# Performance work log

Measured on AMD Instinct MI355X. Metric: run time of the kernel, lower is better.

The kernel has to match this reference:

```python
import jax, jax.numpy as jnp
import numpy as np

NUM_TAGS = 64
SEQ_LEN = 512
BATCH = 512


def setup_inputs() -> dict:
    key = jax.random.key(0)
    k1, k2, k3, k4, k5 = jax.random.split(key, 5)
    emissions = jax.random.normal(k1, (SEQ_LEN, BATCH, NUM_TAGS), dtype=jnp.float32)
    tags = jax.random.randint(k2, (SEQ_LEN, BATCH), 0, NUM_TAGS, dtype=jnp.int32)
    mask = jnp.ones((SEQ_LEN, BATCH), dtype=jnp.int32)
    start_transitions = jax.random.uniform(k3, (NUM_TAGS,), dtype=jnp.float32)
    end_transitions = jax.random.uniform(k4, (NUM_TAGS,), dtype=jnp.float32)
    transitions = jax.random.uniform(k5, (NUM_TAGS, NUM_TAGS), dtype=jnp.float32)
    return {
        "emissions": emissions,
        "tags": tags,
        "mask": mask,
        "start_transitions": start_transitions,
        "end_transitions": end_transitions,
        "transitions": transitions,
    }


def _compute_score(emissions, tags, mask, start_transitions, end_transitions, transitions):
    # emissions: (S,B,T), tags/mask: (S,B)
    seq_length, batch_size = tags.shape
    maskf = mask.astype(jnp.float32)
    barange = jnp.arange(batch_size)
    # emission scores for gold tags at every step: (S,B)
    emit = jnp.take_along_axis(emissions, tags[:, :, None], axis=2)[:, :, 0]
    # transition scores between consecutive gold tags: (S-1,B)
    trans = transitions[tags[:-1], tags[1:]]
    score = start_transitions[tags[0]] + emit[0]
    score = score + ((trans + emit[1:]) * maskf[1:]).sum(axis=0)
    seq_ends = mask.astype(jnp.int32).sum(axis=0) - 1  # (B,)
    last_tags = tags[seq_ends, barange]
    score = score + end_transitions[last_tags]
    return score  # (B,)


def _compute_normalizer(emissions, mask, start_transitions, end_transitions, transitions):
    # sequential forward-algorithm scan over time
    score0 = start_transitions + emissions[0]  # (B,T)

    def step(score, inp):
        em, m = inp  # em: (B,T), m: (B,)
        # (B,Tprev,Tnext) logsumexp over Tprev
        next_score = jax.nn.logsumexp(
            score[:, :, None] + transitions[None, :, :] + em[:, None, :], axis=1
        )
        score = jnp.where(m[:, None].astype(bool), next_score, score)
        return score, None

    score, _ = jax.lax.scan(step, score0, (emissions[1:], mask[1:]))
    return jax.nn.logsumexp(score + end_transitions, axis=1)  # (B,)


def reference(emissions, tags, mask, start_transitions, end_transitions, transitions):
    numerator = _compute_score(emissions, tags, mask, start_transitions, end_transitions, transitions)
    denominator = _compute_normalizer(emissions, mask, start_transitions, end_transitions, transitions)
    llh = numerator - denominator
    return llh.sum()  # reduction='sum'
```

## Files before the change

### kernel.cpp

```cpp
#include <hip/hip_runtime.h>

#define T   512
#define B   512
#define NT  64
#define QS  16
#define NQ  (T / QS)
#define RING 4

typedef _Float16 h2 __attribute__((ext_vector_type(2)));

__device__ __forceinline__ float rflf(float x) {
    return __uint_as_float(__builtin_amdgcn_readfirstlane(__float_as_uint(x)));
}

__device__ __forceinline__ float dot2(h2 a, h2 b, float c) {
#if __has_builtin(__builtin_amdgcn_fdot2)
    return __builtin_amdgcn_fdot2(a, b, c, false);
#else
    return c + (float)a.x * (float)b.x + (float)a.y * (float)b.y;
#endif
}

__device__ __forceinline__ h2 bch2(int u) { return __builtin_bit_cast(h2, u); }

__global__ __launch_bounds__(64) void crf_fused(
    const float* __restrict__ emissions,
    const int*   __restrict__ tags,
    const int*   __restrict__ mask,
    const float* __restrict__ startT,
    const float* __restrict__ endT,
    const float* __restrict__ trans,
    float* __restrict__ out)
{
    const int j = threadIdx.x;

    __shared__ __align__(16) float ebuf[RING][QS][NT];

    if (blockIdx.x < B) {
        const int b = blockIdx.x;

        h2 Eh[NT / 2];
#pragma unroll
        for (int m = 0; m < NT / 2; ++m) {
            Eh[m].x = (_Float16)__expf(trans[(2 * m)     * NT + j]);
            Eh[m].y = (_Float16)__expf(trans[(2 * m + 1) * NT + j]);
        }

        const int jr = j >> 4;
        const int c0 = (j & 15) * 4;
        float4 sA[4];

        auto issue_q = [&](int g) {
#pragma unroll
            for (int k = 0; k < 4; ++k) {
                const int t = g * QS + 4 * k + jr;
                sA[k] = *(const float4*)&emissions[((size_t)t * B + b) * NT + c0];
            }
        };
        auto write_q = [&](int g) {
#pragma unroll
            for (int k = 0; k < 4; ++k) {
                float4 w;
                w.x = __expf(sA[k].x); w.y = __expf(sA[k].y);
                w.z = __expf(sA[k].z); w.w = __expf(sA[k].w);
                *(float4*)&ebuf[g & (RING - 1)][4 * k + jr][c0] = w;
            }
        };

        for (int g = 0; g < 3; ++g) { issue_q(g); write_q(g); }
        issue_q(3);

        const float e0  = emissions[(size_t)b * NT + j];
        const float sc0 = startT[j] + e0;
        const float S0  = rflf(sc0);
        float q = __expf(sc0 - S0);
        int   K = 0;

        int pk_i;
        {
            const int qi = __float_as_int(q);
            const int qo = __builtin_amdgcn_update_dpp(0, qi, 0xB1, 0xF, 0xF, true);
            pk_i = __builtin_bit_cast(int,
                    __builtin_amdgcn_cvt_pkrtz(q, __int_as_float(qo)));
        }

        float* eflat = &ebuf[0][0][0];
        int bits_prev;
        int mpre = mask[j * B + b];
        unsigned long long mbc = 0;

        {
            int u[32];
#pragma unroll
            for (int n = 0; n < 32; ++n)
                u[n] = __builtin_amdgcn_readlane(pk_i, 2 * n);
            float a[8] = {0.f, 0.f, 0.f, 0.f, 0.f, 0.f, 0.f, 0.f};
#pragma unroll
            for (int n = 0; n < 32; ++n)
                a[n & 7] = dot2(bch2(u[n]), Eh[n], a[n & 7]);
            const float p = ((a[0] + a[1]) + (a[2] + a[3]))
                          + ((a[4] + a[5]) + (a[6] + a[7]));
            bits_prev = __builtin_amdgcn_readfirstlane(__float_as_int(p));
            const int  k = ((bits_prev >> 23) & 255) - 127;
            const float r = __int_as_float((125 - k) << 23);
            const float X1 = eflat[NT + j];
            const int  m1 = mask[B + b];
            if (m1) { q = (p * X1) * r; K = k + 2; }
            const int qo = __builtin_amdgcn_update_dpp(0, __float_as_int(q),
                                                       0xB1, 0xF, 0xF, true);
            pk_i = __builtin_bit_cast(int,
                    __builtin_amdgcn_cvt_pkrtz(q, __int_as_float(qo)));
        }

        float Xc = eflat[2 * NT + j];
        float Xn = eflat[3 * NT + j];

        auto stepF = [&](int s) {
            int u[32];
#pragma unroll
            for (int n = 0; n < 32; ++n)
                u[n] = __builtin_amdgcn_readlane(pk_i, 2 * n);
            __builtin_amdgcn_sched_barrier(0);
            const int  k = ((bits_prev >> 23) & 255) - 127;
            const float r = __int_as_float((125 - k) << 23);
            K += k + 2;
            float a[8] = {0.f, 0.f, 0.f, 0.f, 0.f, 0.f, 0.f, 0.f};
#pragma unroll
            for (int n = 0; n < 32; ++n)
                a[n & 7] = dot2(bch2(u[n]), Eh[n], a[n & 7]);
            const float sXr = Xc * r;
            const float p = ((a[0] + a[1]) + (a[2] + a[3]))
                          + ((a[4] + a[5]) + (a[6] + a[7]));
            q = p * sXr;
            bits_prev = __builtin_amdgcn_readfirstlane(__float_as_int(p));
            const int qo = __builtin_amdgcn_update_dpp(0, __float_as_int(q),
                                                       0xB1, 0xF, 0xF, true);
            pk_i = __builtin_bit_cast(int,
                    __builtin_amdgcn_cvt_pkrtz(q, __int_as_float(qo)));
            Xc = Xn;
            Xn = eflat[((s + 2) & 63) * NT + j];
        };

        auto stepM = [&](int s) {
            int u[32];
#pragma unroll
            for (int n = 0; n < 32; ++n)
                u[n] = __builtin_amdgcn_readlane(pk_i, 2 * n);
            __builtin_amdgcn_sched_barrier(0);
            const int  k = ((bits_prev >> 23) & 255) - 127;
            const float r = __int_as_float((125 - k) << 23);
            const bool mc = (mbc >> (s & 63)) & 1ull;
            const float mf = mc ? 1.0f : 0.0f;
            K += mc ? (k + 2) : 0;
            float a[8] = {0.f, 0.f, 0.f, 0.f, 0.f, 0.f, 0.f, 0.f};
#pragma unroll
            for (int n = 0; n < 32; ++n)
                a[n & 7] = dot2(bch2(u[n]), Eh[n], a[n & 7]);
            const float sXr = Xc * r;
            const float p = ((a[0] + a[1]) + (a[2] + a[3]))
                          + ((a[4] + a[5]) + (a[6] + a[7]));
            const float qn = p * sXr;
            q = fmaf(mf, qn - q, q);
            bits_prev = __builtin_amdgcn_readfirstlane(__float_as_int(p));
            const int qo = __builtin_amdgcn_update_dpp(0, __float_as_int(q),
                                                       0xB1, 0xF, 0xF, true);
            pk_i = __builtin_bit_cast(int,
                    __builtin_amdgcn_cvt_pkrtz(q, __int_as_float(qo)));
            Xc = Xn;
            Xn = eflat[((s + 2) & 63) * NT + j];
        };

        for (int x = 0; x < NQ; ++x) {
            const int gw = (x + 3 < NQ) ? x + 3 : NQ - 1;
            write_q(gw);
            const int gl = (x + 4 < NQ) ? x + 4 : NQ - 1;
            issue_q(gl);

            if ((x & 3) == 0) {
                mbc = __ballot(mpre != 0);
                const int cn = ((x >> 2) + 1 < 8) ? (x >> 2) + 1 : 7;
                mpre = mask[(cn * 64 + j) * B + b];
            }

            const unsigned qb = (unsigned)(mbc >> ((x & 3) << 4)) & 0xFFFFu;
            const int tt0 = (x == 0) ? 2 : 0;

            if (qb == 0xFFFFu) {
#pragma unroll 1
                for (int tt = tt0; tt < QS; ++tt) stepF(x * QS + tt);
            } else {
#pragma unroll 1
                for (int tt = tt0; tt < QS; ++tt) stepM(x * QS + tt);
            }
        }

        float v = q * __expf(endT[j]);
#pragma unroll
        for (int off = 32; off > 0; off >>= 1)
            v += __shfl_xor(v, off);
        if (j == 0)
            atomicAdd(out, -(S0 + (float)K * 0.69314718f + __logf(v)));

    } else {
        const int b = blockIdx.x - B;

        float acc = 0.f;
        int   cnt = 0;
#pragma unroll
        for (int m = 0; m < T / 64; ++m) {
            const int t  = j + 64 * m;
            const int mv = mask[t * B + b];
            const int tg = tags[t * B + b];
            cnt += (int)__popcll(__ballot(mv != 0));
            if (t == 0) {
                acc += startT[tg] + emissions[(size_t)b * NT + tg];
            } else if (mv) {
                const int tp = tags[(t - 1) * B + b];
                acc += trans[tp * NT + tg]
                     + emissions[(size_t)(t * B + b) * NT + tg];
            }
        }
#pragma unroll
        for (int off = 32; off > 0; off >>= 1)
            acc += __shfl_xor(acc, off);
        if (j == 0) {
            const int last = tags[(size_t)(cnt - 1) * B + b];
            atomicAdd(out, acc + endT[last]);
        }
    }
}

extern "C" void kernel_launch(void* const* d_in, const int* in_sizes, int n_in,
                              void* d_out, int out_size, void* d_ws, size_t ws_size,
                              hipStream_t stream) {
    const float* emissions = (const float*)d_in[0];
    const int*   tags      = (const int*)  d_in[1];
    const int*   mask      = (const int*)  d_in[2];
    const float* startT    = (const float*)d_in[3];
    const float* endT      = (const float*)d_in[4];
    const float* trans     = (const float*)d_in[5];
    float* out = (float*)d_out;

    hipMemsetAsync(out, 0, sizeof(float), stream);
    crf_fused<<<2 * B, 64, 0, stream>>>(
        emissions, tags, mask, startT, endT, trans, out);
}
```

Before: 193.4 us.

## Split forward scan into forward/backward halves meeting at midpoint

```diff
diff --git a/kernel.cpp b/kernel.cpp
--- a/kernel.cpp
+++ b/kernel.cpp
@@ -5,6 +5,7 @@
 #define NT  64
 #define QS  16
 #define NQ  (T / QS)
+#define FNQ 16
 #define RING 4
 
 typedef _Float16 h2 __attribute__((ext_vector_type(2)));
@@ -12,7 +13,6 @@
 __device__ __forceinline__ float rflf(float x) {
     return __uint_as_float(__builtin_amdgcn_readfirstlane(__float_as_uint(x)));
 }
-
 __device__ __forceinline__ float dot2(h2 a, h2 b, float c) {
 #if __has_builtin(__builtin_amdgcn_fdot2)
     return __builtin_amdgcn_fdot2(a, b, c, false);
@@ -20,20 +20,25 @@
     return c + (float)a.x * (float)b.x + (float)a.y * (float)b.y;
 #endif
 }
-
-__device__ __forceinline__ h2 bch2(int u) { return __builtin_bit_cast(h2, u); }
-
-__global__ __launch_bounds__(64) void crf_fused(
+__device__ __forceinline__ h2  bch2(int u) { return __builtin_bit_cast(h2, u); }
+__device__ __forceinline__ int cvtpk(float a, float b) {
+    return __builtin_bit_cast(int, __builtin_amdgcn_cvt_pkrtz(a, b));
+}
+
+__global__ __launch_bounds__(64) void crf_main(
     const float* __restrict__ emissions,
     const int*   __restrict__ tags,
     const int*   __restrict__ mask,
     const float* __restrict__ startT,
     const float* __restrict__ endT,
     const float* __restrict__ trans,
+    float* __restrict__ wqf,
+    float* __restrict__ wqb,
+    float* __restrict__ wsf,
+    float* __restrict__ wsb,
     float* __restrict__ out)
 {
     const int j = threadIdx.x;
-
     __shared__ __align__(16) float ebuf[RING][QS][NT];
 
     if (blockIdx.x < B) {
@@ -49,7 +54,6 @@
         const int jr = j >> 4;
         const int c0 = (j & 15) * 4;
         float4 sA[4];
-
         auto issue_q = [&](int g) {
 #pragma unroll
             for (int k = 0; k < 4; ++k) {
@@ -66,7 +70,6 @@
                 *(float4*)&ebuf[g & (RING - 1)][4 * k + jr][c0] = w;
             }
         };
-
         for (int g = 0; g < 3; ++g) { issue_q(g); write_q(g); }
         issue_q(3);
 
@@ -75,15 +78,12 @@
         const float S0  = rflf(sc0);
         float q = __expf(sc0 - S0);
         int   K = 0;
-
         int pk_i;
         {
             const int qi = __float_as_int(q);
             const int qo = __builtin_amdgcn_update_dpp(0, qi, 0xB1, 0xF, 0xF, true);
-            pk_i = __builtin_bit_cast(int,
-                    __builtin_amdgcn_cvt_pkrtz(q, __int_as_float(qo)));
-        }
-
+            pk_i = cvtpk(q, __int_as_float(qo));
+        }
         float* eflat = &ebuf[0][0][0];
         int bits_prev;
         int mpre = mask[j * B + b];
@@ -92,100 +92,80 @@
         {
             int u[32];
 #pragma unroll
-            for (int n = 0; n < 32; ++n)
-                u[n] = __builtin_amdgcn_readlane(pk_i, 2 * n);
-            float a[8] = {0.f, 0.f, 0.f, 0.f, 0.f, 0.f, 0.f, 0.f};
-#pragma unroll
-            for (int n = 0; n < 32; ++n)
-                a[n & 7] = dot2(bch2(u[n]), Eh[n], a[n & 7]);
-            const float p = ((a[0] + a[1]) + (a[2] + a[3]))
-                          + ((a[4] + a[5]) + (a[6] + a[7]));
+            for (int m = 0; m < 32; ++m) u[m] = __builtin_amdgcn_readlane(pk_i, 2 * m);
+            float a[8] = {0.f,0.f,0.f,0.f,0.f,0.f,0.f,0.f};
+#pragma unroll
+            for (int m = 0; m < 32; ++m) a[m & 7] = dot2(bch2(u[m]), Eh[m], a[m & 7]);
+            const float p = ((a[0]+a[1])+(a[2]+a[3])) + ((a[4]+a[5])+(a[6]+a[7]));
             bits_prev = __builtin_amdgcn_readfirstlane(__float_as_int(p));
             const int  k = ((bits_prev >> 23) & 255) - 127;
             const float r = __int_as_float((125 - k) << 23);
             const float X1 = eflat[NT + j];
             const int  m1 = mask[B + b];
             if (m1) { q = (p * X1) * r; K = k + 2; }
-            const int qo = __builtin_amdgcn_update_dpp(0, __float_as_int(q),
-                                                       0xB1, 0xF, 0xF, true);
-            pk_i = __builtin_bit_cast(int,
-                    __builtin_amdgcn_cvt_pkrtz(q, __int_as_float(qo)));
-        }
-
+            const int qo = __builtin_amdgcn_update_dpp(0, __float_as_int(q), 0xB1, 0xF, 0xF, true);
+            pk_i = cvtpk(q, __int_as_float(qo));
+        }
         float Xc = eflat[2 * NT + j];
         float Xn = eflat[3 * NT + j];
 
         auto stepF = [&](int s) {
             int u[32];
 #pragma unroll
-            for (int n = 0; n < 32; ++n)
-                u[n] = __builtin_amdgcn_readlane(pk_i, 2 * n);
+            for (int m = 0; m < 32; ++m) u[m] = __builtin_amdgcn_readlane(pk_i, 2 * m);
             __builtin_amdgcn_sched_barrier(0);
             const int  k = ((bits_prev >> 23) & 255) - 127;
             const float r = __int_as_float((125 - k) << 23);
             K += k + 2;
-            float a[8] = {0.f, 0.f, 0.f, 0.f, 0.f, 0.f, 0.f, 0.f};
-#pragma unroll
-            for (int n = 0; n < 32; ++n)
-                a[n & 7] = dot2(bch2(u[n]), Eh[n], a[n & 7]);
+            float a[8] = {0.f,0.f,0.f,0.f,0.f,0.f,0.f,0.f};
+#pragma unroll
+            for (int m = 0; m < 32; ++m) a[m & 7] = dot2(bch2(u[m]), Eh[m], a[m & 7]);
             const float sXr = Xc * r;
-            const float p = ((a[0] + a[1]) + (a[2] + a[3]))
-                          + ((a[4] + a[5]) + (a[6] + a[7]));
+            const float p = ((a[0]+a[1])+(a[2]+a[3])) + ((a[4]+a[5])+(a[6]+a[7]));
             q = p * sXr;
             bits_prev = __builtin_amdgcn_readfirstlane(__float_as_int(p));
-            const int qo = __builtin_amdgcn_update_dpp(0, __float_as_int(q),
-                                                       0xB1, 0xF, 0xF, true);
-            pk_i = __builtin_bit_cast(int,
-                    __builtin_amdgcn_cvt_pkrtz(q, __int_as_float(qo)));
+            const int qo = __builtin_amdgcn_update_dpp(0, __float_as_int(q), 0xB1, 0xF, 0xF, true);
+            pk_i = cvtpk(q, __int_as_float(qo));
             Xc = Xn;
             Xn = eflat[((s + 2) & 63) * NT + j];
         };
-
         auto stepM = [&](int s) {
             int u[32];
 #pragma unroll
-            for (int n = 0; n < 32; ++n)
-                u[n] = __builtin_amdgcn_readlane(pk_i, 2 * n);
+            for (int m = 0; m < 32; ++m) u[m] = __builtin_amdgcn_readlane(pk_i, 2 * m);
             __builtin_amdgcn_sched_barrier(0);
             const int  k = ((bits_prev >> 23) & 255) - 127;
             const float r = __int_as_float((125 - k) << 23);
             const bool mc = (mbc >> (s & 63)) & 1ull;
             const float mf = mc ? 1.0f : 0.0f;
             K += mc ? (k + 2) : 0;
-            float a[8] = {0.f, 0.f, 0.f, 0.f, 0.f, 0.f, 0.f, 0.f};
-#pragma unroll
-            for (int n = 0; n < 32; ++n)
-                a[n & 7] = dot2(bch2(u[n]), Eh[n], a[n & 7]);
+            float a[8] = {0.f,0.f,0.f,0.f,0.f,0.f,0.f,0.f};
+#pragma unroll
+            for (int m = 0; m < 32; ++m) a[m & 7] = dot2(bch2(u[m]), Eh[m], a[m & 7]);
             const float sXr = Xc * r;
-            const float p = ((a[0] + a[1]) + (a[2] + a[3]))
-                          + ((a[4] + a[5]) + (a[6] + a[7]));
+            const float p = ((a[0]+a[1])+(a[2]+a[3])) + ((a[4]+a[5])+(a[6]+a[7]));
             const float qn = p * sXr;
             q = fmaf(mf, qn - q, q);
             bits_prev = __builtin_amdgcn_readfirstlane(__float_as_int(p));
-            const int qo = __builtin_amdgcn_update_dpp(0, __float_as_int(q),
-                                                       0xB1, 0xF, 0xF, true);
-            pk_i = __builtin_bit_cast(int,
-                    __builtin_amdgcn_cvt_pkrtz(q, __int_as_float(qo)));
+            const int qo = __builtin_amdgcn_update_dpp(0, __float_as_int(q), 0xB1, 0xF, 0xF, true);
+            pk_i = cvtpk(q, __int_as_float(qo));
             Xc = Xn;
             Xn = eflat[((s + 2) & 63) * NT + j];
         };
 
-        for (int x = 0; x < NQ; ++x) {
-            const int gw = (x + 3 < NQ) ? x + 3 : NQ - 1;
+        for (int x = 0; x < FNQ; ++x) {
+            const int gw = (x + 3 < FNQ) ? x + 3 : FNQ - 1;
             write_q(gw);
-            const int gl = (x + 4 < NQ) ? x + 4 : NQ - 1;
+            const int gl = (x + 4 < FNQ) ? x + 4 : FNQ - 1;
             issue_q(gl);
-
             if ((x & 3) == 0) {
                 mbc = __ballot(mpre != 0);
-                const int cn = ((x >> 2) + 1 < 8) ? (x >> 2) + 1 : 7;
+                const int cn = ((x >> 2) + 1 < 4) ? (x >> 2) + 1 : 3;
                 mpre = mask[(cn * 64 + j) * B + b];
             }
-
-            const unsigned qb = (unsigned)(mbc >> ((x & 3) << 4)) & 0xFFFFu;
+            const unsigned qb16 = (unsigned)(mbc >> ((x & 3) << 4)) & 0xFFFFu;
             const int tt0 = (x == 0) ? 2 : 0;
-
-            if (qb == 0xFFFFu) {
+            if (qb16 == 0xFFFFu) {
 #pragma unroll 1
                 for (int tt = tt0; tt < QS; ++tt) stepF(x * QS + tt);
             } else {
@@ -193,17 +173,138 @@
                 for (int tt = tt0; tt < QS; ++tt) stepM(x * QS + tt);
             }
         }
-
-        float v = q * __expf(endT[j]);
-#pragma unroll
-        for (int off = 32; off > 0; off >>= 1)
-            v += __shfl_xor(v, off);
-        if (j == 0)
-            atomicAdd(out, -(S0 + (float)K * 0.69314718f + __logf(v)));
+        wqf[b * 64 + j] = q;
+        if (j == 0) wsf[b] = S0 + (float)K * 0.69314718f;
+
+    } else if (blockIdx.x < 2 * B) {
+        const int b = blockIdx.x - B;
+
+        h2 Er[NT / 2];
+#pragma unroll
+        for (int m = 0; m < NT / 2; ++m) {
+            Er[m].x = (_Float16)__expf(trans[j * NT + 2 * m]);
+            Er[m].y = (_Float16)__expf(trans[j * NT + 2 * m + 1]);
+        }
+
+        const int jr = j >> 4;
+        const int c0 = (j & 15) * 4;
+        float4 sA[4];
+        auto issue_q = [&](int g) {
+#pragma unroll
+            for (int k = 0; k < 4; ++k) {
+                const int t = g * QS + 4 * k + jr;
+                sA[k] = *(const float4*)&emissions[((size_t)t * B + b) * NT + c0];
+            }
+        };
+        auto write_q = [&](int g) {
+#pragma unroll
+            for (int k = 0; k < 4; ++k) {
+                float4 w;
+                w.x = __expf(sA[k].x); w.y = __expf(sA[k].y);
+                w.z = __expf(sA[k].z); w.w = __expf(sA[k].w);
+                *(float4*)&ebuf[g & (RING - 1)][4 * k + jr][c0] = w;
+            }
+        };
+        for (int g = 31; g > 28; --g) { issue_q(g); write_q(g); }
+        issue_q(28);
+
+        float v = __expf(endT[j]);
+        int   K = 0;
+        float* eflat = &ebuf[0][0][0];
+        int bits_prev;
+        int mpre = mask[(7 * 64 + j) * B + b];
+        unsigned long long mbc = 0;
+        int pk_i;
+        {
+            const float y  = v * eflat[63 * NT + j];
+            const int  yo = __builtin_amdgcn_update_dpp(0, __float_as_int(y), 0xB1, 0xF, 0xF, true);
+            pk_i = cvtpk(y, __int_as_float(yo));
+        }
+        {
+            int u[32];
+#pragma unroll
+            for (int m = 0; m < 32; ++m) u[m] = __builtin_amdgcn_readlane(pk_i, 2 * m);
+            float a[8] = {0.f,0.f,0.f,0.f,0.f,0.f,0.f,0.f};
+#pragma unroll
+            for (int m = 0; m < 32; ++m) a[m & 7] = dot2(bch2(u[m]), Er[m], a[m & 7]);
+            const float p = ((a[0]+a[1])+(a[2]+a[3])) + ((a[4]+a[5])+(a[6]+a[7]));
+            bits_prev = __builtin_amdgcn_readfirstlane(__float_as_int(p));
+            const int  k = ((bits_prev >> 23) & 255) - 127;
+            const float r = __int_as_float((125 - k) << 23);
+            const int  m511 = mask[511 * B + b];
+            if (m511) { v = p * r; K = k + 2; }
+            const float y  = v * eflat[62 * NT + j];
+            const int  yo = __builtin_amdgcn_update_dpp(0, __float_as_int(y), 0xB1, 0xF, 0xF, true);
+            pk_i = cvtpk(y, __int_as_float(yo));
+        }
+
+        auto bstepF = [&](int s) {
+            int u[32];
+#pragma unroll
+            for (int m = 0; m < 32; ++m) u[m] = __builtin_amdgcn_readlane(pk_i, 2 * m);
+            __builtin_amdgcn_sched_barrier(0);
+            const int  k = ((bits_prev >> 23) & 255) - 127;
+            const float r = __int_as_float((125 - k) << 23);
+            K += k + 2;
+            float a[8] = {0.f,0.f,0.f,0.f,0.f,0.f,0.f,0.f};
+#pragma unroll
+            for (int m = 0; m < 32; ++m) a[m & 7] = dot2(bch2(u[m]), Er[m], a[m & 7]);
+            const float Xn = eflat[((s - 1) & 63) * NT + j];
+            const float p = ((a[0]+a[1])+(a[2]+a[3])) + ((a[4]+a[5])+(a[6]+a[7]));
+            v = p * r;
+            bits_prev = __builtin_amdgcn_readfirstlane(__float_as_int(p));
+            const float y  = v * Xn;
+            const int  yo = __builtin_amdgcn_update_dpp(0, __float_as_int(y), 0xB1, 0xF, 0xF, true);
+            pk_i = cvtpk(y, __int_as_float(yo));
+        };
+        auto bstepM = [&](int s) {
+            int u[32];
+#pragma unroll
+            for (int m = 0; m < 32; ++m) u[m] = __builtin_amdgcn_readlane(pk_i, 2 * m);
+            __builtin_amdgcn_sched_barrier(0);
+            const int  k = ((bits_prev >> 23) & 255) - 127;
+            const float r = __int_as_float((125 - k) << 23);
+            const bool mc = (mbc >> (s & 63)) & 1ull;
+            const float mf = mc ? 1.0f : 0.0f;
+            K += mc ? (k + 2) : 0;
+            float a[8] = {0.f,0.f,0.f,0.f,0.f,0.f,0.f,0.f};
+#pragma unroll
+            for (int m = 0; m < 32; ++m) a[m & 7] = dot2(bch2(u[m]), Er[m], a[m & 7]);
+            const float Xn = eflat[((s - 1) & 63) * NT + j];
+            const float p = ((a[0]+a[1])+(a[2]+a[3])) + ((a[4]+a[5])+(a[6]+a[7]));
+            const float vn = p * r;
+            v = fmaf(mf, vn - v, v);
+            bits_prev = __builtin_amdgcn_readfirstlane(__float_as_int(p));
+            const float y  = v * Xn;
+            const int  yo = __builtin_amdgcn_update_dpp(0, __float_as_int(y), 0xB1, 0xF, 0xF, true);
+            pk_i = cvtpk(y, __int_as_float(yo));
+        };
+
+        for (int x = NQ - 1; x >= 16; --x) {
+            const int gw = (x - 3 >= 16) ? x - 3 : 16;
+            write_q(gw);
+            const int gl = (x - 4 >= 16) ? x - 4 : 16;
+            issue_q(gl);
+            if ((x & 3) == 3) {
+                mbc = __ballot(mpre != 0);
+                const int cn = ((x >> 2) - 1 > 4) ? (x >> 2) - 1 : 4;
+                mpre = mask[(cn * 64 + j) * B + b];
+            }
+            const unsigned qb16 = (unsigned)(mbc >> ((x & 3) << 4)) & 0xFFFFu;
+            const int tts = (x == NQ - 1) ? QS - 2 : QS - 1;
+            if (qb16 == 0xFFFFu) {
+#pragma unroll 1
+                for (int tt = tts; tt >= 0; --tt) bstepF(x * QS + tt);
+            } else {
+#pragma unroll 1
+                for (int tt = tts; tt >= 0; --tt) bstepM(x * QS + tt);
+            }
+        }
+        wqb[b * 64 + j] = v;
+        if (j == 0) wsb[b] = (float)K * 0.69314718f;
 
     } else {
-        const int b = blockIdx.x - B;
-
+        const int b = blockIdx.x - 2 * B;
         float acc = 0.f;
         int   cnt = 0;
 #pragma unroll
@@ -230,6 +331,191 @@
     }
 }
 
+__global__ __launch_bounds__(64) void crf_comb(
+    const float* __restrict__ wqf, const float* __restrict__ wqb,
+    const float* __restrict__ wsf, const float* __restrict__ wsb,
+    float* __restrict__ out)
+{
+    const int b = blockIdx.x;
+    const int j = threadIdx.x;
+    float v = wqf[b * 64 + j] * wqb[b * 64 + j];
+#pragma unroll
+    for (int off = 32; off > 0; off >>= 1)
+        v += __shfl_xor(v, off);
+    if (j == 0)
+        atomicAdd(out, -(wsf[b] + wsb[b] + __logf(v)));
+}
+
+__global__ __launch_bounds__(64) void crf_fused(
+    const float* __restrict__ emissions,
+    const int*   __restrict__ tags,
+    const int*   __restrict__ mask,
+    const float* __restrict__ startT,
+    const float* __restrict__ endT,
+    const float* __restrict__ trans,
+    float* __restrict__ out)
+{
+    const int j = threadIdx.x;
+    __shared__ __align__(16) float ebuf[RING][QS][NT];
+
+    if (blockIdx.x < B) {
+        const int b = blockIdx.x;
+        h2 Eh[NT / 2];
+#pragma unroll
+        for (int m = 0; m < NT / 2; ++m) {
+            Eh[m].x = (_Float16)__expf(trans[(2 * m)     * NT + j]);
+            Eh[m].y = (_Float16)__expf(trans[(2 * m + 1) * NT + j]);
+        }
+        const int jr = j >> 4;
+        const int c0 = (j & 15) * 4;
+        float4 sA[4];
+        auto issue_q = [&](int g) {
+#pragma unroll
+            for (int k = 0; k < 4; ++k) {
+                const int t = g * QS + 4 * k + jr;
+                sA[k] = *(const float4*)&emissions[((size_t)t * B + b) * NT + c0];
+            }
+        };
+        auto write_q = [&](int g) {
+#pragma unroll
+            for (int k = 0; k < 4; ++k) {
+                float4 w;
+                w.x = __expf(sA[k].x); w.y = __expf(sA[k].y);
+                w.z = __expf(sA[k].z); w.w = __expf(sA[k].w);
+                *(float4*)&ebuf[g & (RING - 1)][4 * k + jr][c0] = w;
+            }
+        };
+        for (int g = 0; g < 3; ++g) { issue_q(g); write_q(g); }
+        issue_q(3);
+
+        const float e0  = emissions[(size_t)b * NT + j];
+        const float sc0 = startT[j] + e0;
+        const float S0  = rflf(sc0);
+        float q = __expf(sc0 - S0);
+        int   K = 0;
+        int pk_i;
+        {
+            const int qi = __float_as_int(q);
+            const int qo = __builtin_amdgcn_update_dpp(0, qi, 0xB1, 0xF, 0xF, true);
+            pk_i = cvtpk(q, __int_as_float(qo));
+        }
+        float* eflat = &ebuf[0][0][0];
+        int bits_prev;
+        int mpre = mask[j * B + b];
+        unsigned long long mbc = 0;
+        {
+            int u[32];
+#pragma unroll
+            for (int m = 0; m < 32; ++m) u[m] = __builtin_amdgcn_readlane(pk_i, 2 * m);
+            float a[8] = {0.f,0.f,0.f,0.f,0.f,0.f,0.f,0.f};
+#pragma unroll
+            for (int m = 0; m < 32; ++m) a[m & 7] = dot2(bch2(u[m]), Eh[m], a[m & 7]);
+            const float p = ((a[0]+a[1])+(a[2]+a[3])) + ((a[4]+a[5])+(a[6]+a[7]));
+            bits_prev = __builtin_amdgcn_readfirstlane(__float_as_int(p));
+            const int  k = ((bits_prev >> 23) & 255) - 127;
+            const float r = __int_as_float((125 - k) << 23);
+            const float X1 = eflat[NT + j];
+            const int  m1 = mask[B + b];
+            if (m1) { q = (p * X1) * r; K = k + 2; }
+            const int qo = __builtin_amdgcn_update_dpp(0, __float_as_int(q), 0xB1, 0xF, 0xF, true);
+            pk_i = cvtpk(q, __int_as_float(qo));
+        }
+        float Xc = eflat[2 * NT + j];
+        float Xn = eflat[3 * NT + j];
+        auto stepF = [&](int s) {
+            int u[32];
+#pragma unroll
+            for (int m = 0; m < 32; ++m) u[m] = __builtin_amdgcn_readlane(pk_i, 2 * m);
+            __builtin_amdgcn_sched_barrier(0);
+            const int  k = ((bits_prev >> 23) & 255) - 127;
+            const float r = __int_as_float((125 - k) << 23);
+            K += k + 2;
+            float a[8] = {0.f,0.f,0.f,0.f,0.f,0.f,0.f,0.f};
+#pragma unroll
+            for (int m = 0; m < 32; ++m) a[m & 7] = dot2(bch2(u[m]), Eh[m], a[m & 7]);
+            const float sXr = Xc * r;
+            const float p = ((a[0]+a[1])+(a[2]+a[3])) + ((a[4]+a[5])+(a[6]+a[7]));
+            q = p * sXr;
+            bits_prev = __builtin_amdgcn_readfirstlane(__float_as_int(p));
+            const int qo = __builtin_amdgcn_update_dpp(0, __float_as_int(q), 0xB1, 0xF, 0xF, true);
+            pk_i = cvtpk(q, __int_as_float(qo));
+            Xc = Xn;
+            Xn = eflat[((s + 2) & 63) * NT + j];
+        };
+        auto stepM = [&](int s) {
+            int u[32];
+#pragma unroll
+            for (int m = 0; m < 32; ++m) u[m] = __builtin_amdgcn_readlane(pk_i, 2 * m);
+            __builtin_amdgcn_sched_barrier(0);
+            const int  k = ((bits_prev >> 23) & 255) - 127;
+            const float r = __int_as_float((125 - k) << 23);
+            const bool mc = (mbc >> (s & 63)) & 1ull;
+            const float mf = mc ? 1.0f : 0.0f;
+            K += mc ? (k + 2) : 0;
+            float a[8] = {0.f,0.f,0.f,0.f,0.f,0.f,0.f,0.f};
+#pragma unroll
+            for (int m = 0; m < 32; ++m) a[m & 7] = dot2(bch2(u[m]), Eh[m], a[m & 7]);
+            const float sXr = Xc * r;
+            const float p = ((a[0]+a[1])+(a[2]+a[3])) + ((a[4]+a[5])+(a[6]+a[7]));
+            const float qn = p * sXr;
+            q = fmaf(mf, qn - q, q);
+            bits_prev = __builtin_amdgcn_readfirstlane(__float_as_int(p));
+            const int qo = __builtin_amdgcn_update_dpp(0, __float_as_int(q), 0xB1, 0xF, 0xF, true);
+            pk_i = cvtpk(q, __int_as_float(qo));
+            Xc = Xn;
+            Xn = eflat[((s + 2) & 63) * NT + j];
+        };
+        for (int x = 0; x < NQ; ++x) {
+            const int gw = (x + 3 < NQ) ? x + 3 : NQ - 1;
+            write_q(gw);
+            const int gl = (x + 4 < NQ) ? x + 4 : NQ - 1;
+            issue_q(gl);
+            if ((x & 3) == 0) {
+                mbc = __ballot(mpre != 0);
+                const int cn = ((x >> 2) + 1 < 8) ? (x >> 2) + 1 : 7;
+                mpre = mask[(cn * 64 + j) * B + b];
+            }
+            const unsigned qb16 = (unsigned)(mbc >> ((x & 3) << 4)) & 0xFFFFu;
+            const int tt0 = (x == 0) ? 2 : 0;
+            if (qb16 == 0xFFFFu) {
+#pragma unroll 1
+                for (int tt = tt0; tt < QS; ++tt) stepF(x * QS + tt);
+            } else {
+#pragma unroll 1
+                for (int tt = tt0; tt < QS; ++tt) stepM(x * QS + tt);
+            }
+        }
+        float v = q * __expf(endT[j]);
+#pragma unroll
+        for (int off = 32; off > 0; off >>= 1) v += __shfl_xor(v, off);
+        if (j == 0)
+            atomicAdd(out, -(S0 + (float)K * 0.69314718f + __logf(v)));
+    } else {
+        const int b = blockIdx.x - B;
+        float acc = 0.f;
+        int   cnt = 0;
+#pragma unroll
+        for (int m = 0; m < T / 64; ++m) {
+            const int t  = j + 64 * m;
+            const int mv = mask[t * B + b];
+            const int tg = tags[t * B + b];
+            cnt += (int)__popcll(__ballot(mv != 0));
+            if (t == 0) {
+                acc += startT[tg] + emissions[(size_t)b * NT + tg];
+            } else if (mv) {
+                const int tp = tags[(t - 1) * B + b];
+                acc += trans[tp * NT + tg] + emissions[(size_t)(t * B + b) * NT + tg];
+            }
+        }
+#pragma unroll
+        for (int off = 32; off > 0; off >>= 1) acc += __shfl_xor(acc, off);
+        if (j == 0) {
+            const int last = tags[(size_t)(cnt - 1) * B + b];
+            atomicAdd(out, acc + endT[last]);
+        }
+    }
+}
+
 extern "C" void kernel_launch(void* const* d_in, const int* in_sizes, int n_in,
                               void* d_out, int out_size, void* d_ws, size_t ws_size,
                               hipStream_t stream) {
@@ -242,6 +528,18 @@
     float* out = (float*)d_out;
 
     hipMemsetAsync(out, 0, sizeof(float), stream);
-    crf_fused<<<2 * B, 64, 0, stream>>>(
-        emissions, tags, mask, startT, endT, trans, out);
-}
+
+    const size_t need = (size_t)(B * 64 * 2 + 2 * B) * sizeof(float);
+    if (d_ws != nullptr && ws_size >= need) {
+        float* wqf = (float*)d_ws;
+        float* wqb = wqf + B * 64;
+        float* wsf = wqb + B * 64;
+        float* wsb = wsf + B;
+        crf_main<<<3 * B, 64, 0, stream>>>(emissions, tags, mask, startT, endT,
+                                           trans, wqf, wqb, wsf, wsb, out);
+        crf_comb<<<B, 64, 0, stream>>>(wqf, wqb, wsf, wsb, out);
+    } else {
+        crf_fused<<<2 * B, 64, 0, stream>>>(emissions, tags, mask, startT,
+                                            endT, trans, out);
+    }
+}
```

Measured after the change: 156.8 us. 1.23x faster.

## Split forward recurrence into concurrent forward and backward halves per batch

Applied to the files above, without the earlier changes.

```diff
diff --git a/kernel.cpp b/kernel.cpp
--- a/kernel.cpp
+++ b/kernel.cpp
@@ -5,6 +5,7 @@
 #define NT  64
 #define QS  16
 #define NQ  (T / QS)
+#define FNQ 16
 #define RING 4
 
 typedef _Float16 h2 __attribute__((ext_vector_type(2)));
@@ -12,7 +13,6 @@
 __device__ __forceinline__ float rflf(float x) {
     return __uint_as_float(__builtin_amdgcn_readfirstlane(__float_as_uint(x)));
 }
-
 __device__ __forceinline__ float dot2(h2 a, h2 b, float c) {
 #if __has_builtin(__builtin_amdgcn_fdot2)
     return __builtin_amdgcn_fdot2(a, b, c, false);
@@ -20,10 +20,12 @@
     return c + (float)a.x * (float)b.x + (float)a.y * (float)b.y;
 #endif
 }
-
-__device__ __forceinline__ h2 bch2(int u) { return __builtin_bit_cast(h2, u); }
-
-__global__ __launch_bounds__(64) void crf_fused(
+__device__ __forceinline__ h2  bch2(int u) { return __builtin_bit_cast(h2, u); }
+__device__ __forceinline__ int cvtpk(float a, float b) {
+    return __builtin_bit_cast(int, __builtin_amdgcn_cvt_pkrtz(a, b));
+}
+
+__global__ __launch_bounds__(128) void crf_all(
     const float* __restrict__ emissions,
     const int*   __restrict__ tags,
     const int*   __restrict__ mask,
@@ -32,24 +34,21 @@
     const float* __restrict__ trans,
     float* __restrict__ out)
 {
-    const int j = threadIdx.x;
-
-    __shared__ __align__(16) float ebuf[RING][QS][NT];
+    const int wid = threadIdx.x >> 6;
+    const int j   = threadIdx.x & 63;
+
+    __shared__ __align__(16) float ebuf2[2][RING][QS][NT];
+    __shared__ float qx[NT];
+    __shared__ float sbb;
 
     if (blockIdx.x < B) {
         const int b = blockIdx.x;
-
-        h2 Eh[NT / 2];
-#pragma unroll
-        for (int m = 0; m < NT / 2; ++m) {
-            Eh[m].x = (_Float16)__expf(trans[(2 * m)     * NT + j]);
-            Eh[m].y = (_Float16)__expf(trans[(2 * m + 1) * NT + j]);
-        }
+        float (*ebuf)[QS][NT] = ebuf2[wid];
+        float* eflat = &ebuf[0][0][0];
 
         const int jr = j >> 4;
         const int c0 = (j & 15) * 4;
         float4 sA[4];
-
         auto issue_q = [&](int g) {
 #pragma unroll
             for (int k = 0; k < 4; ++k) {
@@ -67,143 +66,240 @@
             }
         };
 
-        for (int g = 0; g < 3; ++g) { issue_q(g); write_q(g); }
-        issue_q(3);
-
-        const float e0  = emissions[(size_t)b * NT + j];
-        const float sc0 = startT[j] + e0;
-        const float S0  = rflf(sc0);
-        float q = __expf(sc0 - S0);
-        int   K = 0;
-
-        int pk_i;
-        {
-            const int qi = __float_as_int(q);
-            const int qo = __builtin_amdgcn_update_dpp(0, qi, 0xB1, 0xF, 0xF, true);
-            pk_i = __builtin_bit_cast(int,
-                    __builtin_amdgcn_cvt_pkrtz(q, __int_as_float(qo)));
+        float qf_final = 0.f, sf_final = 0.f;
+
+        if (wid == 0) {
+            h2 Eh[NT / 2];
+#pragma unroll
+            for (int m = 0; m < NT / 2; ++m) {
+                Eh[m].x = (_Float16)__expf(trans[(2 * m)     * NT + j]);
+                Eh[m].y = (_Float16)__expf(trans[(2 * m + 1) * NT + j]);
+            }
+
+            for (int g = 0; g < 3; ++g) { issue_q(g); write_q(g); }
+            issue_q(3);
+
+            const float e0  = emissions[(size_t)b * NT + j];
+            const float sc0 = startT[j] + e0;
+            const float S0  = rflf(sc0);
+            float q = __expf(sc0 - S0);
+            int   K = 0;
+            int pk_i;
+            {
+                const int qi = __float_as_int(q);
+                const int qo = __builtin_amdgcn_update_dpp(0, qi, 0xB1, 0xF, 0xF, true);
+                pk_i = cvtpk(q, __int_as_float(qo));
+            }
+            int bits_prev;
+            int mpre = mask[j * B + b];
+            unsigned long long mbc = 0;
+
+            {
+                int u[32];
+#pragma unroll
+                for (int m = 0; m < 32; ++m) u[m] = __builtin_amdgcn_readlane(pk_i, 2 * m);
+                float a[8] = {0.f,0.f,0.f,0.f,0.f,0.f,0.f,0.f};
+#pragma unroll
+                for (int m = 0; m < 32; ++m) a[m & 7] = dot2(bch2(u[m]), Eh[m], a[m & 7]);
+                const float p = ((a[0]+a[1])+(a[2]+a[3])) + ((a[4]+a[5])+(a[6]+a[7]));
+                bits_prev = __builtin_amdgcn_readfirstlane(__float_as_int(p));
+                const int  k = ((bits_prev >> 23) & 255) - 127;
+                const float r = __int_as_float((125 - k) << 23);
+                const float X1 = eflat[NT + j];
+                const int  m1 = mask[B + b];
+                if (m1) { q = (p * X1) * r; K = k + 2; }
+                const int qo = __builtin_amdgcn_update_dpp(0, __float_as_int(q), 0xB1, 0xF, 0xF, true);
+                pk_i = cvtpk(q, __int_as_float(qo));
+            }
+            float Xc = eflat[2 * NT + j];
+            float Xn = eflat[3 * NT + j];
+
+            auto stepF = [&](int s) {
+                int u[32];
+#pragma unroll
+                for (int m = 0; m < 32; ++m) u[m] = __builtin_amdgcn_readlane(pk_i, 2 * m);
+                __builtin_amdgcn_sched_barrier(0);
+                const int  k = ((bits_prev >> 23) & 255) - 127;
+                const float r = __int_as_float((125 - k) << 23);
+                K += k + 2;
+                float a[8] = {0.f,0.f,0.f,0.f,0.f,0.f,0.f,0.f};
+#pragma unroll
+                for (int m = 0; m < 32; ++m) a[m & 7] = dot2(bch2(u[m]), Eh[m], a[m & 7]);
+                const float sXr = Xc * r;
+                const float p = ((a[0]+a[1])+(a[2]+a[3])) + ((a[4]+a[5])+(a[6]+a[7]));
+                q = p * sXr;
+                bits_prev = __builtin_amdgcn_readfirstlane(__float_as_int(p));
+                const int qo = __builtin_amdgcn_update_dpp(0, __float_as_int(q), 0xB1, 0xF, 0xF, true);
+                pk_i = cvtpk(q, __int_as_float(qo));
+                Xc = Xn;
+                Xn = eflat[((s + 2) & 63) * NT + j];
+            };
+            auto stepM = [&](int s) {
+                int u[32];
+#pragma unroll
+                for (int m = 0; m < 32; ++m) u[m] = __builtin_amdgcn_readlane(pk_i, 2 * m);
+                __builtin_amdgcn_sched_barrier(0);
+                const int  k = ((bits_prev >> 23) & 255) - 127;
+                const float r = __int_as_float((125 - k) << 23);
+                const bool mc = (mbc >> (s & 63)) & 1ull;
+                const float mf = mc ? 1.0f : 0.0f;
+                K += mc ? (k + 2) : 0;
+                float a[8] = {0.f,0.f,0.f,0.f,0.f,0.f,0.f,0.f};
+#pragma unroll
+                for (int m = 0; m < 32; ++m) a[m & 7] = dot2(bch2(u[m]), Eh[m], a[m & 7]);
+                const float sXr = Xc * r;
+                const float p = ((a[0]+a[1])+(a[2]+a[3])) + ((a[4]+a[5])+(a[6]+a[7]));
+                const float qn = p * sXr;
+                q = fmaf(mf, qn - q, q);
+                bits_prev = __builtin_amdgcn_readfirstlane(__float_as_int(p));
+                const int qo = __builtin_amdgcn_update_dpp(0, __float_as_int(q), 0xB1, 0xF, 0xF, true);
+                pk_i = cvtpk(q, __int_as_float(qo));
+                Xc = Xn;
+                Xn = eflat[((s + 2) & 63) * NT + j];
+            };
+
+            for (int x = 0; x < FNQ; ++x) {
+                const int gw = (x + 3 < FNQ) ? x + 3 : FNQ - 1;
+                write_q(gw);
+                const int gl = (x + 4 < FNQ) ? x + 4 : FNQ - 1;
+                issue_q(gl);
+                if ((x & 3) == 0) {
+                    mbc = __ballot(mpre != 0);
+                    const int cn = ((x >> 2) + 1 < 4) ? (x >> 2) + 1 : 3;
+                    mpre = mask[(cn * 64 + j) * B + b];
+                }
+                const unsigned qb16 = (unsigned)(mbc >> ((x & 3) << 4)) & 0xFFFFu;
+                const int tt0 = (x == 0) ? 2 : 0;
+                if (qb16 == 0xFFFFu) {
+#pragma unroll 1
+                    for (int tt = tt0; tt < QS; ++tt) stepF(x * QS + tt);
+                } else {
+#pragma unroll 1
+                    for (int tt = tt0; tt < QS; ++tt) stepM(x * QS + tt);
+                }
+            }
+            qf_final = q;
+            sf_final = S0 + (float)K * 0.69314718f;
+
+        } else {
+            h2 Er[NT / 2];
+#pragma unroll
+            for (int m = 0; m < NT / 2; ++m) {
+                Er[m].x = (_Float16)__expf(trans[j * NT + 2 * m]);
+                Er[m].y = (_Float16)__expf(trans[j * NT + 2 * m + 1]);
+            }
+
+            for (int g = 31; g > 28; --g) { issue_q(g); write_q(g); }
+            issue_q(28);
+
+            float v = __expf(endT[j]);
+            int   K = 0;
+            int bits_prev;
+            int mpre = mask[(7 * 64 + j) * B + b];
+            unsigned long long mbc = 0;
+            int pk_i;
+            {
+                const float y  = v * eflat[63 * NT + j];
+                const int  yo = __builtin_amdgcn_update_dpp(0, __float_as_int(y), 0xB1, 0xF, 0xF, true);
+                pk_i = cvtpk(y, __int_as_float(yo));
+            }
+            {
+                int u[32];
+#pragma unroll
+                for (int m = 0; m < 32; ++m) u[m] = __builtin_amdgcn_readlane(pk_i, 2 * m);
+                float a[8] = {0.f,0.f,0.f,0.f,0.f,0.f,0.f,0.f};
+#pragma unroll
+                for (int m = 0; m < 32; ++m) a[m & 7] = dot2(bch2(u[m]), Er[m], a[m & 7]);
+                const float p = ((a[0]+a[1])+(a[2]+a[3])) + ((a[4]+a[5])+(a[6]+a[7]));
+                bits_prev = __builtin_amdgcn_readfirstlane(__float_as_int(p));
+                const int  k = ((bits_prev >> 23) & 255) - 127;
+                const float r = __int_as_float((125 - k) << 23);
+                const int  m511 = mask[511 * B + b];
+                if (m511) { v = p * r; K = k + 2; }
+                const float y  = v * eflat[62 * NT + j];
+                const int  yo = __builtin_amdgcn_update_dpp(0, __float_as_int(y), 0xB1, 0xF, 0xF, true);
+                pk_i = cvtpk(y, __int_as_float(yo));
+            }
+
+            auto bstepF = [&](int s) {
+                int u[32];
+#pragma unroll
+                for (int m = 0; m < 32; ++m) u[m] = __builtin_amdgcn_readlane(pk_i, 2 * m);
+                __builtin_amdgcn_sched_barrier(0);
+                const int  k = ((bits_prev >> 23) & 255) - 127;
+                const float r = __int_as_float((125 - k) << 23);
+                K += k + 2;
+                float a[8] = {0.f,0.f,0.f,0.f,0.f,0.f,0.f,0.f};
+#pragma unroll
+                for (int m = 0; m < 32; ++m) a[m & 7] = dot2(bch2(u[m]), Er[m], a[m & 7]);
+                const float Xn = eflat[((s - 1) & 63) * NT + j];
+                const float p = ((a[0]+a[1])+(a[2]+a[3])) + ((a[4]+a[5])+(a[6]+a[7]));
+                v = p * r;
+                bits_prev = __builtin_amdgcn_readfirstlane(__float_as_int(p));
+                const float y  = v * Xn;
+                const int  yo = __builtin_amdgcn_update_dpp(0, __float_as_int(y), 0xB1, 0xF, 0xF, true);
+                pk_i = cvtpk(y, __int_as_float(yo));
+            };
+            auto bstepM = [&](int s) {
+                int u[32];
+#pragma unroll
+                for (int m = 0; m < 32; ++m) u[m] = __builtin_amdgcn_readlane(pk_i, 2 * m);
+                __builtin_amdgcn_sched_barrier(0);
+                const int  k = ((bits_prev >> 23) & 255) - 127;
+                const float r = __int_as_float((125 - k) << 23);
+                const bool mc = (mbc >> (s & 63)) & 1ull;
+                const float mf = mc ? 1.0f : 0.0f;
+                K += mc ? (k + 2) : 0;
+                float a[8] = {0.f,0.f,0.f,0.f,0.f,0.f,0.f,0.f};
+#pragma unroll
+                for (int m = 0; m < 32; ++m) a[m & 7] = dot2(bch2(u[m]), Er[m], a[m & 7]);
+                const float Xn = eflat[((s - 1) & 63) * NT + j];
+                const float p = ((a[0]+a[1])+(a[2]+a[3])) + ((a[4]+a[5])+(a[6]+a[7]));
+                const float vn = p * r;
+                v = fmaf(mf, vn - v, v);
+                bits_prev = __builtin_amdgcn_readfirstlane(__float_as_int(p));
+                const float y  = v * Xn;
+                const int  yo = __builtin_amdgcn_update_dpp(0, __float_as_int(y), 0xB1, 0xF, 0xF, true);
+                pk_i = cvtpk(y, __int_as_float(yo));
+            };
+
+            for (int x = NQ - 1; x >= 16; --x) {
+                const int gw = (x - 3 >= 16) ? x - 3 : 16;
+                write_q(gw);
+                const int gl = (x - 4 >= 16) ? x - 4 : 16;
+                issue_q(gl);
+                if ((x & 3) == 3) {
+                    mbc = __ballot(mpre != 0);
+                    const int cn = ((x >> 2) - 1 > 4) ? (x >> 2) - 1 : 4;
+                    mpre = mask[(cn * 64 + j) * B + b];
+                }
+                const unsigned qb16 = (unsigned)(mbc >> ((x & 3) << 4)) & 0xFFFFu;
+                const int tts = (x == NQ - 1) ? QS - 2 : QS - 1;
+                if (qb16 == 0xFFFFu) {
+#pragma unroll 1
+                    for (int tt = tts; tt >= 0; --tt) bstepF(x * QS + tt);
+                } else {
+#pragma unroll 1
+                    for (int tt = tts; tt >= 0; --tt) bstepM(x * QS + tt);
+                }
+            }
+            qx[j] = v;
+            if (j == 0) sbb = (float)K * 0.69314718f;
         }
 
-        float* eflat = &ebuf[0][0][0];
-        int bits_prev;
-        int mpre = mask[j * B + b];
-        unsigned long long mbc = 0;
-
-        {
-            int u[32];
-#pragma unroll
-            for (int n = 0; n < 32; ++n)
-                u[n] = __builtin_amdgcn_readlane(pk_i, 2 * n);
-            float a[8] = {0.f, 0.f, 0.f, 0.f, 0.f, 0.f, 0.f, 0.f};
-#pragma unroll
-            for (int n = 0; n < 32; ++n)
-                a[n & 7] = dot2(bch2(u[n]), Eh[n], a[n & 7]);
-            const float p = ((a[0] + a[1]) + (a[2] + a[3]))
-                          + ((a[4] + a[5]) + (a[6] + a[7]));
-            bits_prev = __builtin_amdgcn_readfirstlane(__float_as_int(p));
-            const int  k = ((bits_prev >> 23) & 255) - 127;
-            const float r = __int_as_float((125 - k) << 23);
-            const float X1 = eflat[NT + j];
-            const int  m1 = mask[B + b];
-            if (m1) { q = (p * X1) * r; K = k + 2; }
-            const int qo = __builtin_amdgcn_update_dpp(0, __float_as_int(q),
-                                                       0xB1, 0xF, 0xF, true);
-            pk_i = __builtin_bit_cast(int,
-                    __builtin_amdgcn_cvt_pkrtz(q, __int_as_float(qo)));
+        __syncthreads();
+
+        if (wid == 0) {
+            float v = qf_final * qx[j];
+#pragma unroll
+            for (int off = 32; off > 0; off >>= 1)
+                v += __shfl_xor(v, off);
+            if (j == 0)
+                atomicAdd(out, -(sf_final + sbb + __logf(v)));
         }
 
-        float Xc = eflat[2 * NT + j];
-        float Xn = eflat[3 * NT + j];
-
-        auto stepF = [&](int s) {
-            int u[32];
-#pragma unroll
-            for (int n = 0; n < 32; ++n)
-                u[n] = __builtin_amdgcn_readlane(pk_i, 2 * n);
-            __builtin_amdgcn_sched_barrier(0);
-            const int  k = ((bits_prev >> 23) & 255) - 127;
-            const float r = __int_as_float((125 - k) << 23);
-            K += k + 2;
-            float a[8] = {0.f, 0.f, 0.f, 0.f, 0.f, 0.f, 0.f, 0.f};
-#pragma unroll
-            for (int n = 0; n < 32; ++n)
-                a[n & 7] = dot2(bch2(u[n]), Eh[n], a[n & 7]);
-            const float sXr = Xc * r;
-            const float p = ((a[0] + a[1]) + (a[2] + a[3]))
-                          + ((a[4] + a[5]) + (a[6] + a[7]));
-            q = p * sXr;
-            bits_prev = __builtin_amdgcn_readfirstlane(__float_as_int(p));
-            const int qo = __builtin_amdgcn_update_dpp(0, __float_as_int(q),
-                                                       0xB1, 0xF, 0xF, true);
-            pk_i = __builtin_bit_cast(int,
-                    __builtin_amdgcn_cvt_pkrtz(q, __int_as_float(qo)));
-            Xc = Xn;
-            Xn = eflat[((s + 2) & 63) * NT + j];
-        };
-
-        auto stepM = [&](int s) {
-            int u[32];
-#pragma unroll
-            for (int n = 0; n < 32; ++n)
-                u[n] = __builtin_amdgcn_readlane(pk_i, 2 * n);
-            __builtin_amdgcn_sched_barrier(0);
-            const int  k = ((bits_prev >> 23) & 255) - 127;
-            const float r = __int_as_float((125 - k) << 23);
-            const bool mc = (mbc >> (s & 63)) & 1ull;
-            const float mf = mc ? 1.0f : 0.0f;
-            K += mc ? (k + 2) : 0;
-            float a[8] = {0.f, 0.f, 0.f, 0.f, 0.f, 0.f, 0.f, 0.f};
-#pragma unroll
-            for (int n = 0; n < 32; ++n)
-                a[n & 7] = dot2(bch2(u[n]), Eh[n], a[n & 7]);
-            const float sXr = Xc * r;
-            const float p = ((a[0] + a[1]) + (a[2] + a[3]))
-                          + ((a[4] + a[5]) + (a[6] + a[7]));
-            const float qn = p * sXr;
-            q = fmaf(mf, qn - q, q);
-            bits_prev = __builtin_amdgcn_readfirstlane(__float_as_int(p));
-            const int qo = __builtin_amdgcn_update_dpp(0, __float_as_int(q),
-                                                       0xB1, 0xF, 0xF, true);
-            pk_i = __builtin_bit_cast(int,
-                    __builtin_amdgcn_cvt_pkrtz(q, __int_as_float(qo)));
-            Xc = Xn;
-            Xn = eflat[((s + 2) & 63) * NT + j];
-        };
-
-        for (int x = 0; x < NQ; ++x) {
-            const int gw = (x + 3 < NQ) ? x + 3 : NQ - 1;
-            write_q(gw);
-            const int gl = (x + 4 < NQ) ? x + 4 : NQ - 1;
-            issue_q(gl);
-
-            if ((x & 3) == 0) {
-                mbc = __ballot(mpre != 0);
-                const int cn = ((x >> 2) + 1 < 8) ? (x >> 2) + 1 : 7;
-                mpre = mask[(cn * 64 + j) * B + b];
-            }
-
-            const unsigned qb = (unsigned)(mbc >> ((x & 3) << 4)) & 0xFFFFu;
-            const int tt0 = (x == 0) ? 2 : 0;
-
-            if (qb == 0xFFFFu) {
-#pragma unroll 1
-                for (int tt = tt0; tt < QS; ++tt) stepF(x * QS + tt);
-            } else {
-#pragma unroll 1
-                for (int tt = tt0; tt < QS; ++tt) stepM(x * QS + tt);
-            }
-        }
-
-        float v = q * __expf(endT[j]);
-#pragma unroll
-        for (int off = 32; off > 0; off >>= 1)
-            v += __shfl_xor(v, off);
-        if (j == 0)
-            atomicAdd(out, -(S0 + (float)K * 0.69314718f + __logf(v)));
-
     } else {
-        const int b = blockIdx.x - B;
-
+        const int b = (blockIdx.x - B) * 2 + wid;
         float acc = 0.f;
         int   cnt = 0;
 #pragma unroll
@@ -242,6 +338,6 @@
     float* out = (float*)d_out;
 
     hipMemsetAsync(out, 0, sizeof(float), stream);
-    crf_fused<<<2 * B, 64, 0, stream>>>(
+    crf_all<<<B + B / 2, 128, 0, stream>>>(
         emissions, tags, mask, startT, endT, trans, out);
 }
```

Measured after the change: 180.8 us. 1.07x faster.
